# Optimization experiments

Measured on AMD Instinct MI355X. Metric: run time of the kernel, lower is better.

## Reference

```python
import jax, jax.numpy as jnp
import numpy as np

B, N, L, ND = 512, 4096, 128, 1


def setup_inputs() -> dict:
    key = jax.random.key(0)
    ks = jax.random.split(key, 20)
    g = lambda k, shape, s=0.05: jax.random.normal(k, shape, dtype=jnp.float32) * s
    IN = 3 * L + ND  # MLP input: [mem, mem, delta_t, x]
    inp = {
        "x": jax.random.normal(ks[0], (B, N, ND), jnp.float32),
        "memory": jax.random.normal(ks[1], (N, L), jnp.float32),
        "delta_t": jax.random.normal(ks[2], (B, N, L), jnp.float32),
        "src_w1": g(ks[3], (L, IN)), "src_b1": g(ks[4], (L,)),
        "src_w2": g(ks[5], (L, L)), "src_b2": g(ks[6], (L,)),
        "tar_w1": g(ks[7], (L, IN)), "tar_b1": g(ks[8], (L,)),
        "tar_w2": g(ks[9], (L, L)), "tar_b2": g(ks[10], (L,)),
        "gru_wih": g(ks[11], (3 * L, L)), "gru_whh": g(ks[12], (3 * L, L)),
        "gru_bih": g(ks[13], (3 * L,)), "gru_bhh": g(ks[14], (3 * L,)),
        "source": jax.random.randint(ks[15], (B, 1), 0, N, dtype=jnp.int64),
        "target": jax.random.randint(ks[16], (B, 1), 0, N, dtype=jnp.int64),
    }
    return inp


def _mlp(h, w1, b1, w2, b2):
    return jax.nn.relu(h @ w1.T + b1) @ w2.T + b2


def _gru_cell(inp, h, wih, whh, bih, bhh):
    gi = inp @ wih.T + bih          # [n, 3L]
    gh = h @ whh.T + bhh            # [n, 3L]
    i_r, i_z, i_n = jnp.split(gi, 3, axis=-1)
    h_r, h_z, h_n = jnp.split(gh, 3, axis=-1)
    r = jax.nn.sigmoid(i_r + h_r)
    z = jax.nn.sigmoid(i_z + h_z)
    n = jnp.tanh(i_n + r * h_n)
    return (1.0 - z) * n + z * h


def reference(x, memory, delta_t, src_w1, src_b1, src_w2, src_b2,
              tar_w1, tar_b1, tar_w2, tar_b2,
              gru_wih, gru_whh, gru_bih, gru_bhh, source, target):
    b = x.shape[0]
    bi = jnp.arange(b)
    s = source[:, 0]
    t = target[:, 0]
    src_mem = memory[s]                 # [B, L]
    tar_mem = memory[t]                 # [B, L]
    src_x = x[bi, s, :]                 # [B, ND]
    tar_x = x[bi, t, :]
    src_dt = delta_t[bi, s, :]          # [B, L]
    tar_dt = delta_t[bi, t, :]
    src_in = jnp.concatenate([src_mem, tar_mem, src_dt, src_x], axis=-1)
    tar_in = jnp.concatenate([tar_mem, src_mem, tar_dt, tar_x], axis=-1)
    src_msg = _mlp(src_in, src_w1, src_b1, src_w2, src_b2)
    tar_msg = _mlp(tar_in, tar_w1, tar_b1, tar_w2, tar_b2)

    # unique + scatter_mean == segment-mean over node ids, touching only seen nodes
    ids = jnp.concatenate([s, t], axis=0)                       # [2B]
    msgs = jnp.concatenate([src_msg, tar_msg], axis=0)          # [2B, L]
    n_nodes = memory.shape[0]
    msg_sum = jax.ops.segment_sum(msgs, ids, num_segments=n_nodes)
    cnt = jax.ops.segment_sum(jnp.ones((ids.shape[0],), msgs.dtype), ids,
                              num_segments=n_nodes)
    agg = msg_sum / jnp.maximum(cnt, 1.0)[:, None]              # [N, L]
    new_mem = _gru_cell(agg, memory, gru_wih, gru_whh, gru_bih, gru_bhh)
    seen = (cnt > 0)[:, None]
    return jnp.where(seen, new_mem, memory)
```

## Files before the change

kernel.cpp:

```cpp
#include <hip/hip_runtime.h>
#include <math.h>

#define BB 512
#define NN 4096
#define LL 128
#define IN_DIM 385
#define NK8_1 49
#define NK8_2 16
#define EPB 2
#define TASKS 1024
#define GPB 4

#define OFF_MSGS  0
#define OFF_HEAD  (OFF_MSGS + TASKS * LL)
#define OFF_NEXT  (OFF_HEAD + NN)
#define OFF_COUNT (OFF_NEXT + TASKS)
#define OFF_LIST  (OFF_COUNT + 4)
#define OFF_W1BS  (OFF_LIST + 1024)
#define OFF_W1BT  (OFF_W1BS + NK8_1 * LL * 4)
#define OFF_W2BS  (OFF_W1BT + NK8_1 * LL * 4)
#define OFF_W2BT  (OFF_W2BS + NK8_2 * LL * 4)
#define OFF_WIHB  (OFF_W2BT + NK8_2 * LL * 4)
#define OFF_WHHB  (OFF_WIHB + 3 * NK8_2 * LL * 4)

__device__ inline unsigned short f2bf(float f) {
    unsigned u = __float_as_uint(f);
    return (unsigned short)((u + 0x7fffu + ((u >> 16) & 1u)) >> 16);
}
__device__ inline unsigned pack2(float lo, float hi) {
    return (unsigned)f2bf(lo) | ((unsigned)f2bf(hi) << 16);
}
struct f8 { float v[8]; };
__device__ inline f8 unpack8(uint4 u) {
    f8 r;
    r.v[0] = __uint_as_float(u.x << 16); r.v[1] = __uint_as_float(u.x & 0xffff0000u);
    r.v[2] = __uint_as_float(u.y << 16); r.v[3] = __uint_as_float(u.y & 0xffff0000u);
    r.v[4] = __uint_as_float(u.z << 16); r.v[5] = __uint_as_float(u.z & 0xffff0000u);
    r.v[6] = __uint_as_float(u.w << 16); r.v[7] = __uint_as_float(u.w & 0xffff0000u);
    return r;
}

__global__ __launch_bounds__(256) void prep_kernel(
    const float* __restrict__ sw1, const float* __restrict__ tw1,
    const float* __restrict__ sw2, const float* __restrict__ tw2,
    const float* __restrict__ wih, const float* __restrict__ whh,
    float* __restrict__ ws)
{
    const int i = blockIdx.x * 256 + threadIdx.x;
    const int stride = gridDim.x * 256;

    int* heads = (int*)ws + OFF_HEAD;
    for (int idx = i; idx < NN; idx += stride)
        heads[idx] = -1;
    if (i == 0)
        ((int*)ws)[OFF_COUNT] = 0;

    uint4* w1bs = (uint4*)(ws + OFF_W1BS);
    uint4* w1bt = (uint4*)(ws + OFF_W1BT);
    for (int idx = i; idx < NK8_1 * LL; idx += stride) {
        const int k8 = idx >> 7, j = idx & 127;
        const int k = k8 * 8;
        float a[8], b[8];
        #pragma unroll
        for (int c = 0; c < 8; ++c) {
            a[c] = (k + c < IN_DIM) ? sw1[j * IN_DIM + k + c] : 0.f;
            b[c] = (k + c < IN_DIM) ? tw1[j * IN_DIM + k + c] : 0.f;
        }
        w1bs[idx] = make_uint4(pack2(a[0], a[1]), pack2(a[2], a[3]),
                               pack2(a[4], a[5]), pack2(a[6], a[7]));
        w1bt[idx] = make_uint4(pack2(b[0], b[1]), pack2(b[2], b[3]),
                               pack2(b[4], b[5]), pack2(b[6], b[7]));
    }
    uint4* w2bs = (uint4*)(ws + OFF_W2BS);
    uint4* w2bt = (uint4*)(ws + OFF_W2BT);
    for (int idx = i; idx < NK8_2 * LL; idx += stride) {
        const int k8 = idx >> 7, j = idx & 127;
        const int k = k8 * 8;
        const float* pa = sw2 + j * LL + k;
        const float* pb = tw2 + j * LL + k;
        w2bs[idx] = make_uint4(pack2(pa[0], pa[1]), pack2(pa[2], pa[3]),
                               pack2(pa[4], pa[5]), pack2(pa[6], pa[7]));
        w2bt[idx] = make_uint4(pack2(pb[0], pb[1]), pack2(pb[2], pb[3]),
                               pack2(pb[4], pb[5]), pack2(pb[6], pb[7]));
    }
    uint4* wihb = (uint4*)(ws + OFF_WIHB);
    uint4* whhb = (uint4*)(ws + OFF_WHHB);
    for (int idx = i; idx < 3 * NK8_2 * LL; idx += stride) {
        const int j = idx & 127;
        const int gk = idx >> 7;
        const int gate = gk >> 4, k8 = gk & 15;
        const float* pa = wih + (gate * LL + j) * LL + k8 * 8;
        const float* pb = whh + (gate * LL + j) * LL + k8 * 8;
        wihb[idx] = make_uint4(pack2(pa[0], pa[1]), pack2(pa[2], pa[3]),
                               pack2(pa[4], pa[5]), pack2(pa[6], pa[7]));
        whhb[idx] = make_uint4(pack2(pb[0], pb[1]), pack2(pb[2], pb[3]),
                               pack2(pb[4], pb[5]), pack2(pb[6], pb[7]));
    }
}

#define BF8_STEP(WU, A0, A1, B0, B1) {                                  \
    const f8 W_ = unpack8(WU);                                          \
    a0 = fmaf(W_.v[0], (A0).x, a0); a1 = fmaf(W_.v[0], (B0).x, a1);     \
    a0 = fmaf(W_.v[1], (A0).y, a0); a1 = fmaf(W_.v[1], (B0).y, a1);     \
    a0 = fmaf(W_.v[2], (A0).z, a0); a1 = fmaf(W_.v[2], (B0).z, a1);     \
    a0 = fmaf(W_.v[3], (A0).w, a0); a1 = fmaf(W_.v[3], (B0).w, a1);     \
    a0 = fmaf(W_.v[4], (A1).x, a0); a1 = fmaf(W_.v[4], (B1).x, a1);     \
    a0 = fmaf(W_.v[5], (A1).y, a0); a1 = fmaf(W_.v[5], (B1).y, a1);     \
    a0 = fmaf(W_.v[6], (A1).z, a0); a1 = fmaf(W_.v[6], (B1).z, a1);     \
    a0 = fmaf(W_.v[7], (A1).w, a0); a1 = fmaf(W_.v[7], (B1).w, a1); }

__global__ __launch_bounds__(256) void edge_msg_kernel(
    const float* __restrict__ x,
    const float* __restrict__ memory,
    const float* __restrict__ delta_t,
    const float* __restrict__ sb1, const float* __restrict__ sb2,
    const float* __restrict__ tb1, const float* __restrict__ tb2,
    const int* __restrict__ source, const int* __restrict__ target,
    float* __restrict__ ws, float* __restrict__ out)
{
    const int tid = threadIdx.x;

    if (blockIdx.x >= 512) {
        const int cb = blockIdx.x - 512;
        float4* out4 = (float4*)out;
        const float4* mem4 = (const float4*)memory;
        for (int idx = cb * 256 + tid; idx < NN * LL / 4; idx += 32 * 256)
            out4[idx] = mem4[idx];
        return;
    }

    const int side  = blockIdx.x & 1;
    const int chunk = blockIdx.x >> 1;
    const int g     = tid >> 7;
    const int j     = tid & 127;

    const int eg0 = chunk * EPB, eg1 = eg0 + 1;
    const int s0 = source[eg0], t0 = target[eg0];
    const int s1 = source[eg1], t1 = target[eg1];
    const int node0  = side ? t0 : s0, other0 = side ? s0 : t0;
    const int node1  = side ? t1 : s1, other1 = side ? s1 : t1;

    __shared__ float h1s[EPB][LL];
    __shared__ float part1[2][EPB][LL];
    __shared__ float part2[2][EPB][LL];

    const uint4* w1b = (const uint4*)(ws + (side ? OFF_W1BT : OFF_W1BS));
    const uint4* w2b = (const uint4*)(ws + (side ? OFF_W2BT : OFF_W2BS));
    const float* b1  = side ? tb1 : sb1;
    const float* b2  = side ? tb2 : sb2;

    {
        float a0 = 0.f, a1 = 0.f;
        const float* nA = memory + (size_t)node0 * LL;
        const float* nB = memory + (size_t)node1 * LL;
        const float* oA = memory + (size_t)other0 * LL;
        const float* oB = memory + (size_t)other1 * LL;
        const float* dA = delta_t + ((size_t)eg0 * NN + node0) * LL;
        const float* dB = delta_t + ((size_t)eg1 * NN + node1) * LL;

        if (g == 0) {
            #pragma unroll 4
            for (int k8 = 0; k8 < 16; ++k8) {
                const uint4 wu = w1b[k8 * LL + j];
                const float4 A0 = *(const float4*)(nA + 8 * k8);
                const float4 A1 = *(const float4*)(nA + 8 * k8 + 4);
                const float4 B0 = *(const float4*)(nB + 8 * k8);
                const float4 B1 = *(const float4*)(nB + 8 * k8 + 4);
                BF8_STEP(wu, A0, A1, B0, B1)
            }
            #pragma unroll 4
            for (int k8 = 16; k8 < 24; ++k8) {
                const uint4 wu = w1b[k8 * LL + j];
                const float4 A0 = *(const float4*)(oA + 8 * k8 - 128);
                const float4 A1 = *(const float4*)(oA + 8 * k8 - 124);
                const float4 B0 = *(const float4*)(oB + 8 * k8 - 128);
                const float4 B1 = *(const float4*)(oB + 8 * k8 - 124);
                BF8_STEP(wu, A0, A1, B0, B1)
            }
        } else {
            #pragma unroll 4
            for (int k8 = 24; k8 < 32; ++k8) {
                const uint4 wu = w1b[k8 * LL + j];
                const float4 A0 = *(const float4*)(oA + 8 * k8 - 128);
                const float4 A1 = *(const float4*)(oA + 8 * k8 - 124);
                const float4 B0 = *(const float4*)(oB + 8 * k8 - 128);
                const float4 B1 = *(const float4*)(oB + 8 * k8 - 124);
                BF8_STEP(wu, A0, A1, B0, B1)
            }
            #pragma unroll 4
            for (int k8 = 32; k8 < 48; ++k8) {
                const uint4 wu = w1b[k8 * LL + j];
                const float4 A0 = *(const float4*)(dA + 8 * k8 - 256);
                const float4 A1 = *(const float4*)(dA + 8 * k8 - 252);
                const float4 B0 = *(const float4*)(dB + 8 * k8 - 256);
                const float4 B1 = *(const float4*)(dB + 8 * k8 - 252);
                BF8_STEP(wu, A0, A1, B0, B1)
            }
            {
                const uint4 wu = w1b[48 * LL + j];
                const float w0 = __uint_as_float(wu.x << 16);
                a0 = fmaf(w0, x[(size_t)eg0 * NN + node0], a0);
                a1 = fmaf(w0, x[(size_t)eg1 * NN + node1], a1);
            }
        }
        part1[g][0][j] = a0;
        part1[g][1][j] = a1;
    }
    __syncthreads();

    h1s[g][j] = fmaxf(part1[0][g][j] + part1[1][g][j] + b1[j], 0.0f);
    __syncthreads();

    {
        const int k80 = g * 8, k81 = k80 + 8;
        float a0 = 0.f, a1 = 0.f;
        #pragma unroll 4
        for (int k8 = k80; k8 < k81; ++k8) {
            const uint4 wu = w2b[k8 * LL + j];
            const float4 A0 = *(const float4*)&h1s[0][8 * k8];
            const float4 A1 = *(const float4*)&h1s[0][8 * k8 + 4];
            const float4 B0 = *(const float4*)&h1s[1][8 * k8];
            const float4 B1 = *(const float4*)&h1s[1][8 * k8 + 4];
            BF8_STEP(wu, A0, A1, B0, B1)
        }
        part2[g][0][j] = a0;
        part2[g][1][j] = a1;
    }
    __syncthreads();

    {
        const int task = side * BB + (g ? eg1 : eg0);
        const float m = part2[0][g][j] + part2[1][g][j] + b2[j];
        ws[OFF_MSGS + (size_t)task * LL + j] = m;
    }
    if (tid < EPB) {
        const int node = tid ? node1 : node0;
        const int task = side * BB + (tid ? eg1 : eg0);
        const int old = atomicExch((int*)ws + OFF_HEAD + node, task);
        ((int*)ws)[OFF_NEXT + task] = old;
        if (old == -1) {
            const int pos = atomicAdd((int*)ws + OFF_COUNT, 1);
            ((int*)ws)[OFF_LIST + pos] = node;
        }
    }
}

__global__ __launch_bounds__(256) void gru_kernel(
    const float* __restrict__ memory,
    const float* __restrict__ bih, const float* __restrict__ bhh,
    const float* __restrict__ ws, float* __restrict__ out)
{
    const int tid = threadIdx.x;
    const int g = tid >> 7, j = tid & 127;
    const int scount = ((const int*)ws)[OFF_COUNT];
    const int base = blockIdx.x * GPB;
    if (base >= scount) return;
    const int nact = min(GPB, scount - base);

    __shared__ float ah[2 * GPB][LL];
    __shared__ float gates[6][GPB][LL];
    __shared__ int   nodes_sh[GPB];

    const int* heads = (const int*)ws + OFF_HEAD;
    const int* nexts = (const int*)ws + OFF_NEXT;

    int nd[GPB];
    #pragma unroll
    for (int s = 0; s < GPB; ++s)
        nd[s] = (base + s < scount) ? ((const int*)ws)[OFF_LIST + base + s]
                                    : ((const int*)ws)[OFF_LIST + base];
    if (tid < GPB) nodes_sh[tid] = nd[tid];

    if (g == 0) {
        #pragma unroll
        for (int s = 0; s < GPB; ++s) {
            float acc = 0.0f;
            int c = 0;
            for (int t = heads[nd[s]]; t != -1; t = nexts[t]) {
                acc += ws[OFF_MSGS + (size_t)t * LL + j];
                ++c;
            }
            ah[s][j] = acc / (float)c;
        }
    } else {
        #pragma unroll
        for (int s = 0; s < GPB; ++s)
            ah[GPB + s][j] = memory[(size_t)nd[s] * LL + j];
    }
    __syncthreads();

    const uint4* wpb = (const uint4*)(ws + (g ? OFF_WHHB : OFF_WIHB));
    float a0[GPB] = {}, a1[GPB] = {}, a2[GPB] = {};
    #pragma unroll 2
    for (int k8 = 0; k8 < NK8_2; ++k8) {
        const f8 w0 = unpack8(wpb[(0 * NK8_2 + k8) * LL + j]);
        const f8 w1 = unpack8(wpb[(1 * NK8_2 + k8) * LL + j]);
        const f8 w2 = unpack8(wpb[(2 * NK8_2 + k8) * LL + j]);
        #pragma unroll
        for (int s = 0; s < GPB; ++s) {
            const float4 v0 = *(const float4*)&ah[g * GPB + s][8 * k8];
            const float4 v1 = *(const float4*)&ah[g * GPB + s][8 * k8 + 4];
            const float v[8] = {v0.x, v0.y, v0.z, v0.w, v1.x, v1.y, v1.z, v1.w};
            #pragma unroll
            for (int c = 0; c < 8; ++c) {
                a0[s] = fmaf(w0.v[c], v[c], a0[s]);
                a1[s] = fmaf(w1.v[c], v[c], a1[s]);
                a2[s] = fmaf(w2.v[c], v[c], a2[s]);
            }
        }
    }
    #pragma unroll
    for (int s = 0; s < GPB; ++s) {
        gates[g * 3 + 0][s][j] = a0[s];
        gates[g * 3 + 1][s][j] = a1[s];
        gates[g * 3 + 2][s][j] = a2[s];
    }
    __syncthreads();

    const int total = nact * LL;
    for (int o = tid; o < total; o += 256) {
        const int s = o >> 7, jj = o & 127;
        const int node = nodes_sh[s];
        const float ir = gates[0][s][jj] + bih[jj];
        const float iz = gates[1][s][jj] + bih[LL + jj];
        const float inn = gates[2][s][jj] + bih[2 * LL + jj];
        const float hr = gates[3][s][jj] + bhh[jj];
        const float hz = gates[4][s][jj] + bhh[LL + jj];
        const float hn = gates[5][s][jj] + bhh[2 * LL + jj];
        const float r = 1.0f / (1.0f + __expf(-(ir + hr)));
        const float z = 1.0f / (1.0f + __expf(-(iz + hz)));
        const float n = tanhf(inn + r * hn);
        const float h = ah[GPB + s][jj];
        out[(size_t)node * LL + jj] = (1.0f - z) * n + z * h;
    }
}

extern "C" void kernel_launch(void* const* d_in, const int* in_sizes, int n_in,
                              void* d_out, int out_size, void* d_ws, size_t ws_size,
                              hipStream_t stream) {
    const float* x        = (const float*)d_in[0];
    const float* memory   = (const float*)d_in[1];
    const float* delta_t  = (const float*)d_in[2];
    const float* src_w1   = (const float*)d_in[3];
    const float* src_b1   = (const float*)d_in[4];
    const float* src_w2   = (const float*)d_in[5];
    const float* src_b2   = (const float*)d_in[6];
    const float* tar_w1   = (const float*)d_in[7];
    const float* tar_b1   = (const float*)d_in[8];
    const float* tar_w2   = (const float*)d_in[9];
    const float* tar_b2   = (const float*)d_in[10];
    const float* gru_wih  = (const float*)d_in[11];
    const float* gru_whh  = (const float*)d_in[12];
    const float* gru_bih  = (const float*)d_in[13];
    const float* gru_bhh  = (const float*)d_in[14];
    const int*   source   = (const int*)d_in[15];
    const int*   target   = (const int*)d_in[16];

    float* out = (float*)d_out;
    float* ws  = (float*)d_ws;

    prep_kernel<<<256, 256, 0, stream>>>(
        src_w1, tar_w1, src_w2, tar_w2, gru_wih, gru_whh, ws);

    edge_msg_kernel<<<544, 256, 0, stream>>>(
        x, memory, delta_t, src_b1, src_b2, tar_b1, tar_b2,
        source, target, ws, out);

    gru_kernel<<<1024 / GPB, 256, 0, stream>>>(
        memory, gru_bih, gru_bhh, ws, out);
}
```

Before: 32.51 us.

## Process four edges per block and move GRU weight packing into edge kernel

Each edge-message block now handles four edges with 512 threads split into four K-groups, so each bf16 weight load is reused across four edge rows, and the block count is halved. Packing of the GRU input and hidden weights moves out of the prep kernel into extra blocks of the edge kernel, which shrinks the prep kernel and its grid. The memory-to-output copy now uses 16 blocks of 512 threads. The trade-offs are higher register pressure, fewer blocks to fill the GPU, and a larger shared-memory reduction.

```diff
diff --git a/kernel.cpp b/kernel.cpp
--- a/kernel.cpp
+++ b/kernel.cpp
@@ -7,7 +7,7 @@
 #define IN_DIM 385
 #define NK8_1 49
 #define NK8_2 16
-#define EPB 2
+#define EPB 4
 #define TASKS 1024
 #define GPB 4
 
@@ -43,7 +43,6 @@
 __global__ __launch_bounds__(256) void prep_kernel(
     const float* __restrict__ sw1, const float* __restrict__ tw1,
     const float* __restrict__ sw2, const float* __restrict__ tw2,
-    const float* __restrict__ wih, const float* __restrict__ whh,
     float* __restrict__ ws)
 {
     const int i = blockIdx.x * 256 + threadIdx.x;
@@ -83,49 +82,66 @@
         w2bt[idx] = make_uint4(pack2(pb[0], pb[1]), pack2(pb[2], pb[3]),
                                pack2(pb[4], pb[5]), pack2(pb[6], pb[7]));
     }
-    uint4* wihb = (uint4*)(ws + OFF_WIHB);
-    uint4* whhb = (uint4*)(ws + OFF_WHHB);
-    for (int idx = i; idx < 3 * NK8_2 * LL; idx += stride) {
-        const int j = idx & 127;
-        const int gk = idx >> 7;
-        const int gate = gk >> 4, k8 = gk & 15;
-        const float* pa = wih + (gate * LL + j) * LL + k8 * 8;
-        const float* pb = whh + (gate * LL + j) * LL + k8 * 8;
-        wihb[idx] = make_uint4(pack2(pa[0], pa[1]), pack2(pa[2], pa[3]),
-                               pack2(pa[4], pa[5]), pack2(pa[6], pa[7]));
-        whhb[idx] = make_uint4(pack2(pb[0], pb[1]), pack2(pb[2], pb[3]),
-                               pack2(pb[4], pb[5]), pack2(pb[6], pb[7]));
-    }
-}
-
-#define BF8_STEP(WU, A0, A1, B0, B1) {                                  \
+}
+
+#define BF8_STEP4(WU, P0, P1, P2, P3, OFS) {                            \
     const f8 W_ = unpack8(WU);                                          \
-    a0 = fmaf(W_.v[0], (A0).x, a0); a1 = fmaf(W_.v[0], (B0).x, a1);     \
-    a0 = fmaf(W_.v[1], (A0).y, a0); a1 = fmaf(W_.v[1], (B0).y, a1);     \
-    a0 = fmaf(W_.v[2], (A0).z, a0); a1 = fmaf(W_.v[2], (B0).z, a1);     \
-    a0 = fmaf(W_.v[3], (A0).w, a0); a1 = fmaf(W_.v[3], (B0).w, a1);     \
-    a0 = fmaf(W_.v[4], (A1).x, a0); a1 = fmaf(W_.v[4], (B1).x, a1);     \
-    a0 = fmaf(W_.v[5], (A1).y, a0); a1 = fmaf(W_.v[5], (B1).y, a1);     \
-    a0 = fmaf(W_.v[6], (A1).z, a0); a1 = fmaf(W_.v[6], (B1).z, a1);     \
-    a0 = fmaf(W_.v[7], (A1).w, a0); a1 = fmaf(W_.v[7], (B1).w, a1); }
-
-__global__ __launch_bounds__(256) void edge_msg_kernel(
+    const float4 A0 = *(const float4*)((P0) + (OFS));                   \
+    const float4 A1 = *(const float4*)((P0) + (OFS) + 4);               \
+    const float4 B0 = *(const float4*)((P1) + (OFS));                   \
+    const float4 B1 = *(const float4*)((P1) + (OFS) + 4);               \
+    const float4 C0 = *(const float4*)((P2) + (OFS));                   \
+    const float4 C1 = *(const float4*)((P2) + (OFS) + 4);               \
+    const float4 D0 = *(const float4*)((P3) + (OFS));                   \
+    const float4 D1 = *(const float4*)((P3) + (OFS) + 4);               \
+    a0 = fmaf(W_.v[0], A0.x, a0); a1 = fmaf(W_.v[0], B0.x, a1);         \
+    a2 = fmaf(W_.v[0], C0.x, a2); a3 = fmaf(W_.v[0], D0.x, a3);         \
+    a0 = fmaf(W_.v[1], A0.y, a0); a1 = fmaf(W_.v[1], B0.y, a1);         \
+    a2 = fmaf(W_.v[1], C0.y, a2); a3 = fmaf(W_.v[1], D0.y, a3);         \
+    a0 = fmaf(W_.v[2], A0.z, a0); a1 = fmaf(W_.v[2], B0.z, a1);         \
+    a2 = fmaf(W_.v[2], C0.z, a2); a3 = fmaf(W_.v[2], D0.z, a3);         \
+    a0 = fmaf(W_.v[3], A0.w, a0); a1 = fmaf(W_.v[3], B0.w, a1);         \
+    a2 = fmaf(W_.v[3], C0.w, a2); a3 = fmaf(W_.v[3], D0.w, a3);         \
+    a0 = fmaf(W_.v[4], A1.x, a0); a1 = fmaf(W_.v[4], B1.x, a1);         \
+    a2 = fmaf(W_.v[4], C1.x, a2); a3 = fmaf(W_.v[4], D1.x, a3);         \
+    a0 = fmaf(W_.v[5], A1.y, a0); a1 = fmaf(W_.v[5], B1.y, a1);         \
+    a2 = fmaf(W_.v[5], C1.y, a2); a3 = fmaf(W_.v[5], D1.y, a3);         \
+    a0 = fmaf(W_.v[6], A1.z, a0); a1 = fmaf(W_.v[6], B1.z, a1);         \
+    a2 = fmaf(W_.v[6], C1.z, a2); a3 = fmaf(W_.v[6], D1.z, a3);         \
+    a0 = fmaf(W_.v[7], A1.w, a0); a1 = fmaf(W_.v[7], B1.w, a1);         \
+    a2 = fmaf(W_.v[7], C1.w, a2); a3 = fmaf(W_.v[7], D1.w, a3); }
+
+__global__ __launch_bounds__(512) void edge_msg_kernel(
     const float* __restrict__ x,
     const float* __restrict__ memory,
     const float* __restrict__ delta_t,
     const float* __restrict__ sb1, const float* __restrict__ sb2,
     const float* __restrict__ tb1, const float* __restrict__ tb2,
+    const float* __restrict__ wih, const float* __restrict__ whh,
     const int* __restrict__ source, const int* __restrict__ target,
     float* __restrict__ ws, float* __restrict__ out)
 {
     const int tid = threadIdx.x;
 
-    if (blockIdx.x >= 512) {
-        const int cb = blockIdx.x - 512;
-        float4* out4 = (float4*)out;
-        const float4* mem4 = (const float4*)memory;
-        for (int idx = cb * 256 + tid; idx < NN * LL / 4; idx += 32 * 256)
-            out4[idx] = mem4[idx];
+    if (blockIdx.x >= 256) {
+        if (blockIdx.x < 272) {
+            const int cb = blockIdx.x - 256;
+            float4* out4 = (float4*)out;
+            const float4* mem4 = (const float4*)memory;
+            for (int idx = cb * 512 + tid; idx < NN * LL / 4; idx += 16 * 512)
+                out4[idx] = mem4[idx];
+        } else {
+            const int idx = (blockIdx.x - 272) * 512 + tid;
+            const int half = idx >= 6144;
+            const int id2 = idx - half * 6144;
+            const int j = id2 & 127;
+            const int gk = id2 >> 7;
+            const int gate = gk >> 4, k8 = gk & 15;
+            const float* p = (half ? whh : wih) + (gate * LL + j) * LL + k8 * 8;
+            uint4* dst = (uint4*)(ws + (half ? OFF_WHHB : OFF_WIHB));
+            dst[id2] = make_uint4(pack2(p[0], p[1]), pack2(p[2], p[3]),
+                                  pack2(p[4], p[5]), pack2(p[6], p[7]));
+        }
         return;
     }
 
@@ -134,108 +150,113 @@
     const int g     = tid >> 7;
     const int j     = tid & 127;
 
-    const int eg0 = chunk * EPB, eg1 = eg0 + 1;
-    const int s0 = source[eg0], t0 = target[eg0];
-    const int s1 = source[eg1], t1 = target[eg1];
-    const int node0  = side ? t0 : s0, other0 = side ? s0 : t0;
-    const int node1  = side ? t1 : s1, other1 = side ? s1 : t1;
+    int eg[EPB], nodev[EPB], otherv[EPB];
+    #pragma unroll
+    for (int e = 0; e < EPB; ++e) {
+        eg[e] = chunk * EPB + e;
+        const int s = source[eg[e]], t = target[eg[e]];
+        nodev[e]  = side ? t : s;
+        otherv[e] = side ? s : t;
+    }
 
     __shared__ float h1s[EPB][LL];
-    __shared__ float part1[2][EPB][LL];
-    __shared__ float part2[2][EPB][LL];
+    __shared__ float part1[4][EPB][LL];
+    __shared__ float part2[4][EPB][LL];
 
     const uint4* w1b = (const uint4*)(ws + (side ? OFF_W1BT : OFF_W1BS));
     const uint4* w2b = (const uint4*)(ws + (side ? OFF_W2BT : OFF_W2BS));
     const float* b1  = side ? tb1 : sb1;
     const float* b2  = side ? tb2 : sb2;
 
+    const float* n0 = memory + (size_t)nodev[0] * LL;
+    const float* n1 = memory + (size_t)nodev[1] * LL;
+    const float* n2 = memory + (size_t)nodev[2] * LL;
+    const float* n3 = memory + (size_t)nodev[3] * LL;
+    const float* o0 = memory + (size_t)otherv[0] * LL;
+    const float* o1 = memory + (size_t)otherv[1] * LL;
+    const float* o2 = memory + (size_t)otherv[2] * LL;
+    const float* o3 = memory + (size_t)otherv[3] * LL;
+    const float* d0 = delta_t + ((size_t)eg[0] * NN + nodev[0]) * LL;
+    const float* d1 = delta_t + ((size_t)eg[1] * NN + nodev[1]) * LL;
+    const float* d2 = delta_t + ((size_t)eg[2] * NN + nodev[2]) * LL;
+    const float* d3 = delta_t + ((size_t)eg[3] * NN + nodev[3]) * LL;
+
     {
-        float a0 = 0.f, a1 = 0.f;
-        const float* nA = memory + (size_t)node0 * LL;
-        const float* nB = memory + (size_t)node1 * LL;
-        const float* oA = memory + (size_t)other0 * LL;
-        const float* oB = memory + (size_t)other1 * LL;
-        const float* dA = delta_t + ((size_t)eg0 * NN + node0) * LL;
-        const float* dB = delta_t + ((size_t)eg1 * NN + node1) * LL;
-
+        float a0 = 0.f, a1 = 0.f, a2 = 0.f, a3 = 0.f;
         if (g == 0) {
             #pragma unroll 4
-            for (int k8 = 0; k8 < 16; ++k8) {
-                const uint4 wu = w1b[k8 * LL + j];
-                const float4 A0 = *(const float4*)(nA + 8 * k8);
-                const float4 A1 = *(const float4*)(nA + 8 * k8 + 4);
-                const float4 B0 = *(const float4*)(nB + 8 * k8);
-                const float4 B1 = *(const float4*)(nB + 8 * k8 + 4);
-                BF8_STEP(wu, A0, A1, B0, B1)
+            for (int k8 = 0; k8 < 12; ++k8) {
+                const uint4 wu = w1b[k8 * LL + j];
+                BF8_STEP4(wu, n0, n1, n2, n3, 8 * k8)
+            }
+        } else if (g == 1) {
+            #pragma unroll 4
+            for (int k8 = 12; k8 < 16; ++k8) {
+                const uint4 wu = w1b[k8 * LL + j];
+                BF8_STEP4(wu, n0, n1, n2, n3, 8 * k8)
             }
             #pragma unroll 4
             for (int k8 = 16; k8 < 24; ++k8) {
                 const uint4 wu = w1b[k8 * LL + j];
-                const float4 A0 = *(const float4*)(oA + 8 * k8 - 128);
-                const float4 A1 = *(const float4*)(oA + 8 * k8 - 124);
-                const float4 B0 = *(const float4*)(oB + 8 * k8 - 128);
-                const float4 B1 = *(const float4*)(oB + 8 * k8 - 124);
-                BF8_STEP(wu, A0, A1, B0, B1)
+                BF8_STEP4(wu, o0, o1, o2, o3, 8 * k8 - 128)
+            }
+        } else if (g == 2) {
+            #pragma unroll 4
+            for (int k8 = 24; k8 < 32; ++k8) {
+                const uint4 wu = w1b[k8 * LL + j];
+                BF8_STEP4(wu, o0, o1, o2, o3, 8 * k8 - 128)
+            }
+            #pragma unroll 4
+            for (int k8 = 32; k8 < 36; ++k8) {
+                const uint4 wu = w1b[k8 * LL + j];
+                BF8_STEP4(wu, d0, d1, d2, d3, 8 * k8 - 256)
             }
         } else {
             #pragma unroll 4
-            for (int k8 = 24; k8 < 32; ++k8) {
-                const uint4 wu = w1b[k8 * LL + j];
-                const float4 A0 = *(const float4*)(oA + 8 * k8 - 128);
-                const float4 A1 = *(const float4*)(oA + 8 * k8 - 124);
-                const float4 B0 = *(const float4*)(oB + 8 * k8 - 128);
-                const float4 B1 = *(const float4*)(oB + 8 * k8 - 124);
-                BF8_STEP(wu, A0, A1, B0, B1)
-            }
-            #pragma unroll 4
-            for (int k8 = 32; k8 < 48; ++k8) {
-                const uint4 wu = w1b[k8 * LL + j];
-                const float4 A0 = *(const float4*)(dA + 8 * k8 - 256);
-                const float4 A1 = *(const float4*)(dA + 8 * k8 - 252);
-                const float4 B0 = *(const float4*)(dB + 8 * k8 - 256);
-                const float4 B1 = *(const float4*)(dB + 8 * k8 - 252);
-                BF8_STEP(wu, A0, A1, B0, B1)
+            for (int k8 = 36; k8 < 48; ++k8) {
+                const uint4 wu = w1b[k8 * LL + j];
+                BF8_STEP4(wu, d0, d1, d2, d3, 8 * k8 - 256)
             }
             {
                 const uint4 wu = w1b[48 * LL + j];
                 const float w0 = __uint_as_float(wu.x << 16);
-                a0 = fmaf(w0, x[(size_t)eg0 * NN + node0], a0);
-                a1 = fmaf(w0, x[(size_t)eg1 * NN + node1], a1);
-            }
-        }
-        part1[g][0][j] = a0;
-        part1[g][1][j] = a1;
-    }
-    __syncthreads();
-
-    h1s[g][j] = fmaxf(part1[0][g][j] + part1[1][g][j] + b1[j], 0.0f);
+                a0 = fmaf(w0, x[(size_t)eg[0] * NN + nodev[0]], a0);
+                a1 = fmaf(w0, x[(size_t)eg[1] * NN + nodev[1]], a1);
+                a2 = fmaf(w0, x[(size_t)eg[2] * NN + nodev[2]], a2);
+                a3 = fmaf(w0, x[(size_t)eg[3] * NN + nodev[3]], a3);
+            }
+        }
+        part1[g][0][j] = a0; part1[g][1][j] = a1;
+        part1[g][2][j] = a2; part1[g][3][j] = a3;
+    }
+    __syncthreads();
+
+    h1s[g][j] = fmaxf(part1[0][g][j] + part1[1][g][j]
+                    + part1[2][g][j] + part1[3][g][j] + b1[j], 0.0f);
     __syncthreads();
 
     {
-        const int k80 = g * 8, k81 = k80 + 8;
-        float a0 = 0.f, a1 = 0.f;
+        const int k80 = g * 4, k81 = k80 + 4;
+        float a0 = 0.f, a1 = 0.f, a2 = 0.f, a3 = 0.f;
         #pragma unroll 4
         for (int k8 = k80; k8 < k81; ++k8) {
             const uint4 wu = w2b[k8 * LL + j];
-            const float4 A0 = *(const float4*)&h1s[0][8 * k8];
-            const float4 A1 = *(const float4*)&h1s[0][8 * k8 + 4];
-            const float4 B0 = *(const float4*)&h1s[1][8 * k8];
-            const float4 B1 = *(const float4*)&h1s[1][8 * k8 + 4];
-            BF8_STEP(wu, A0, A1, B0, B1)
-        }
-        part2[g][0][j] = a0;
-        part2[g][1][j] = a1;
+            BF8_STEP4(wu, &h1s[0][0], &h1s[1][0], &h1s[2][0], &h1s[3][0], 8 * k8)
+        }
+        part2[g][0][j] = a0; part2[g][1][j] = a1;
+        part2[g][2][j] = a2; part2[g][3][j] = a3;
     }
     __syncthreads();
 
     {
-        const int task = side * BB + (g ? eg1 : eg0);
-        const float m = part2[0][g][j] + part2[1][g][j] + b2[j];
+        const int task = side * BB + eg[g];
+        const float m = part2[0][g][j] + part2[1][g][j]
+                      + part2[2][g][j] + part2[3][g][j] + b2[j];
         ws[OFF_MSGS + (size_t)task * LL + j] = m;
     }
     if (tid < EPB) {
-        const int node = tid ? node1 : node0;
-        const int task = side * BB + (tid ? eg1 : eg0);
+        const int node = nodev[tid];
+        const int task = side * BB + eg[tid];
         const int old = atomicExch((int*)ws + OFF_HEAD + node, task);
         ((int*)ws)[OFF_NEXT + task] = old;
         if (old == -1) {
@@ -359,12 +380,12 @@
     float* out = (float*)d_out;
     float* ws  = (float*)d_ws;
 
-    prep_kernel<<<256, 256, 0, stream>>>(
-        src_w1, tar_w1, src_w2, tar_w2, gru_wih, gru_whh, ws);
-
-    edge_msg_kernel<<<544, 256, 0, stream>>>(
+    prep_kernel<<<128, 256, 0, stream>>>(
+        src_w1, tar_w1, src_w2, tar_w2, ws);
+
+    edge_msg_kernel<<<296, 512, 0, stream>>>(
         x, memory, delta_t, src_b1, src_b2, tar_b1, tar_b2,
-        source, target, ws, out);
+        gru_wih, gru_whh, source, target, ws, out);
 
     gru_kernel<<<1024 / GPB, 256, 0, stream>>>(
         memory, gru_bih, gru_bhh, ws, out);
```

Result: faster. 30.65 us (-5.8%).
